# Performance work log

Hardware: AMD Instinct MI355X
Metric: run time of the kernel (lower is better)

## Reference

```python
import jax, jax.numpy as jnp
import numpy as np

B, H, S, DH = 2, 16, 2048, 64
MASK_FILL = -10000.0


def setup_inputs() -> dict:
    key = jax.random.key(0)
    kq, kk, kv = jax.random.split(key, 3)
    q = jax.random.normal(kq, (B, H, S, DH), dtype=jnp.float32)
    k = jax.random.normal(kk, (B, H, S, DH), dtype=jnp.float32)
    v = jax.random.normal(kv, (B, H, S, DH), dtype=jnp.float32)
    # causal mask: True where attention is disallowed (upper triangle)
    mask = jnp.triu(jnp.ones((S, S), dtype=jnp.bool_), k=1)
    return {"q": q, "k": k, "v": v, "mask": mask}


def reference(q, k, v, mask):
    scale = 1.0 / jnp.sqrt(jnp.asarray(k.shape[-1], dtype=q.dtype))
    # scores: [B, H, S_q, S_k]
    scores = jnp.einsum("bhqd,bhkd->bhqk", q, k) * scale
    # additive mask: masked_fill on a zeros [S_k, S_v] matrix -> -10000 where mask
    attn_bias = jnp.where(mask, jnp.asarray(MASK_FILL, dtype=k.dtype),
                          jnp.asarray(0.0, dtype=k.dtype))
    scores = scores + attn_bias  # broadcast over batch/heads
    attn = jax.nn.softmax(scores, axis=-1)
    # dropout_rate = 0.0 -> identity
    return jnp.einsum("bhqk,bhkd->bhqd", attn, v)
```

## Files before the change

kernel.cpp:

```cpp
#include <hip/hip_runtime.h>


#define S_LEN  2048
#define DHDIM  64
#define NHEADS 32
#define LDP    72
#define M2     23.083120654223414f
#define QSCALE 0.18033688011117658f

typedef __attribute__((ext_vector_type(8))) short bf16x8;
typedef __attribute__((ext_vector_type(4))) float f32x4;

__device__ __forceinline__ unsigned short f2bf(float f) {
    unsigned u = __float_as_uint(f);
    return (unsigned short)((u + 0x7fffu + ((u >> 16) & 1u)) >> 16);
}
__device__ __forceinline__ void ld8(const float* p, float* f) {
    float4 a = *(const float4*)p, b = *(const float4*)(p + 4);
    f[0]=a.x; f[1]=a.y; f[2]=a.z; f[3]=a.w; f[4]=b.x; f[5]=b.y; f[6]=b.z; f[7]=b.w;
}
__device__ __forceinline__ uint4 pack8(const float* f, float scale) {
    union { uint4 v; unsigned short s[8]; } w;
    #pragma unroll
    for (int j = 0; j < 8; j++) w.s[j] = f2bf(f[j] * scale);
    return w.v;
}
__device__ __forceinline__ unsigned packhi(float a, float b) {
#if __has_builtin(__builtin_amdgcn_perm)
    return __builtin_amdgcn_perm(__float_as_uint(b), __float_as_uint(a), 0x07060302u);
#else
    return (__float_as_uint(a) >> 16) | (__float_as_uint(b) & 0xffff0000u);
#endif
}

__global__ __launch_bounds__(256) void prep(
    const float* __restrict__ Qf, const float* __restrict__ Kf,
    const float* __restrict__ Vf, unsigned short* __restrict__ qb,
    unsigned short* __restrict__ kb, unsigned short* __restrict__ vtb)
{
    const int st = blockIdx.x, bh = blockIdx.y;
    __shared__ unsigned short lt[64][LDP];
    const float* vp = Vf + ((size_t)bh * S_LEN + st * 64) * DHDIM;
    for (int c = threadIdx.x; c < 512; c += 256) {
        int s = c >> 3, d0 = (c & 7) * 8;
        float f[8]; ld8(vp + s * DHDIM + d0, f);
        #pragma unroll
        for (int j = 0; j < 8; j++) lt[d0 + j][s] = f2bf(f[j]);
    }
    size_t off = ((size_t)(bh * 32 + st) * 4096) + (size_t)threadIdx.x * 16;
    float f[8];
    ld8(Qf + off, f);     *(uint4*)(qb + off)     = pack8(f, QSCALE);
    ld8(Qf + off + 8, f); *(uint4*)(qb + off + 8) = pack8(f, QSCALE);
    ld8(Kf + off, f);     *(uint4*)(kb + off)     = pack8(f, 1.0f);
    ld8(Kf + off + 8, f); *(uint4*)(kb + off + 8) = pack8(f, 1.0f);
    __syncthreads();
    unsigned short* op = vtb + (size_t)bh * DHDIM * S_LEN + st * 64;
    for (int c = threadIdx.x; c < 512; c += 256) {
        int d = c >> 3, s0 = (c & 7) * 8;
        *(uint4*)(op + (size_t)d * S_LEN + s0) = *(const uint4*)&lt[d][s0];
    }
}

template <bool PRE>
__global__ __launch_bounds__(256) void fattn_kernel(
    const void* __restrict__ Qp, const void* __restrict__ Kp,
    const void* __restrict__ Vp, float* __restrict__ O)
{
    __shared__ unsigned short smem[192 * LDP];
    unsigned short (*ks)[LDP]  = (unsigned short(*)[LDP])smem;
    unsigned short (*vts)[LDP] = (unsigned short(*)[LDP])(smem + 64 * LDP);
    unsigned short (*qs)[LDP]  = (unsigned short(*)[LDP])(smem + 128 * LDP);
    unsigned short (*pst)[LDP] = qs;

    const int id = blockIdx.y * 32 + blockIdx.x;
    const int g  = id >> 8;
    const int r8 = id & 255;
    const int bh = r8 >> 3;
    const int s8 = r8 & 7;
    const int qt = (g == 0) ? 31 - 2 * s8
                 : (g == 1) ? 2 * s8
                 : (g == 2) ? 30 - 2 * s8
                            : 2 * s8 + 1;

    const int tid = threadIdx.x;
    const int wave = tid >> 6, lane = tid & 63;
    const int quad = lane >> 4, l16 = lane & 15;

    if constexpr (PRE) {
        const unsigned short* src = (const unsigned short*)Qp
            + ((size_t)bh * S_LEN + qt * 64) * DHDIM;
        for (int c = tid; c < 512; c += 256) {
            int row = c >> 3, c8 = (c & 7) * 8;
            *(uint4*)&qs[row][c8] = *(const uint4*)(src + row * DHDIM + c8);
        }
    } else {
        const float* src = (const float*)Qp + ((size_t)bh * S_LEN + qt * 64) * DHDIM;
        for (int c = tid; c < 512; c += 256) {
            int row = c >> 3, c8 = (c & 7) * 8;
            float f[8]; ld8(src + row * DHDIM + c8, f);
            *(uint4*)&qs[row][c8] = pack8(f, QSCALE);
        }
    }
    __syncthreads();

    const int prow = wave * 16 + l16;
    const bf16x8 bq0 = *(const bf16x8*)&qs[prow][quad * 8];
    const bf16x8 bq1 = *(const bf16x8*)&qs[prow][32 + quad * 8];

    float l_p = 0.f;
    f32x4 of[4];
    #pragma unroll
    for (int n = 0; n < 4; n++) of[n] = (f32x4){0.f, 0.f, 0.f, 0.f};

    for (int kt = 0; kt <= qt; kt++) {
        __syncthreads();

        if constexpr (PRE) {
            const unsigned short* ksrc = (const unsigned short*)Kp
                + ((size_t)bh * S_LEN + kt * 64) * DHDIM;
            const unsigned short* vsrc = (const unsigned short*)Vp
                + (size_t)bh * DHDIM * S_LEN + kt * 64;
            for (int c = tid; c < 512; c += 256) {
                int row = c >> 3, c8 = (c & 7) * 8;
                *(uint4*)&ks[row][c8]  = *(const uint4*)(ksrc + row * DHDIM + c8);
                *(uint4*)&vts[row][c8] = *(const uint4*)(vsrc + (size_t)row * S_LEN + c8);
            }
        } else {
            const float* ksrc = (const float*)Kp + ((size_t)bh * S_LEN + kt * 64) * DHDIM;
            const float* vsrc = (const float*)Vp + ((size_t)bh * S_LEN + kt * 64) * DHDIM;
            for (int c = tid; c < 512; c += 256) {
                int row = c >> 3, c8 = (c & 7) * 8;
                float f[8];
                ld8(ksrc + row * DHDIM + c8, f);
                *(uint4*)&ks[row][c8] = pack8(f, 1.0f);
                ld8(vsrc + row * DHDIM + c8, f);
                #pragma unroll
                for (int j = 0; j < 8; j++) vts[c8 + j][row] = f2bf(f[j]);
            }
        }
        __syncthreads();

        f32x4 sf[4];
        #pragma unroll
        for (int n = 0; n < 4; n++) {
            bf16x8 ak0 = *(const bf16x8*)&ks[n * 16 + l16][quad * 8];
            bf16x8 ak1 = *(const bf16x8*)&ks[n * 16 + l16][32 + quad * 8];
            sf[n] = (f32x4){-M2, -M2, -M2, -M2};
            sf[n] = __builtin_amdgcn_mfma_f32_16x16x32_bf16(ak0, bq0, sf[n], 0, 0, 0);
            sf[n] = __builtin_amdgcn_mfma_f32_16x16x32_bf16(ak1, bq1, sf[n], 0, 0, 0);
        }

        const bool diag = (kt == qt);
        #pragma unroll
        for (int n = 0; n < 4; n++) {
            float p[4];
            #pragma unroll
            for (int r = 0; r < 4; r++) {
                p[r] = exp2f(sf[n][r]);
                if (diag && (n * 16 + quad * 4 + r > wave * 16 + l16)) p[r] = 0.f;
                l_p += p[r];
            }
            uint2 dw;
            dw.x = packhi(p[0], p[1]);
            dw.y = packhi(p[2], p[3]);
            *(uint2*)&pst[prow][n * 16 + quad * 4] = dw;
        }
        asm volatile("s_waitcnt lgkmcnt(0)" ::: "memory");

        bf16x8 bp0 = *(const bf16x8*)&pst[prow][quad * 8];
        bf16x8 bp1 = *(const bf16x8*)&pst[prow][32 + quad * 8];
        #pragma unroll
        for (int n = 0; n < 4; n++) {
            bf16x8 av0 = *(const bf16x8*)&vts[n * 16 + l16][quad * 8];
            bf16x8 av1 = *(const bf16x8*)&vts[n * 16 + l16][32 + quad * 8];
            of[n] = __builtin_amdgcn_mfma_f32_16x16x32_bf16(av0, bp0, of[n], 0, 0, 0);
            of[n] = __builtin_amdgcn_mfma_f32_16x16x32_bf16(av1, bp1, of[n], 0, 0, 0);
        }
    }

    l_p += __shfl_xor(l_p, 16);
    l_p += __shfl_xor(l_p, 32);
    const float inv = 1.f / l_p;
    float* op = O + ((size_t)bh * S_LEN + qt * 64 + wave * 16 + l16) * DHDIM;
    #pragma unroll
    for (int n = 0; n < 4; n++) {
        float4 o4 = make_float4(of[n][0] * inv, of[n][1] * inv,
                                of[n][2] * inv, of[n][3] * inv);
        *(float4*)(op + n * 16 + quad * 4) = o4;
    }
}

extern "C" void kernel_launch(void* const* d_in, const int* in_sizes, int n_in,
                              void* d_out, int out_size, void* d_ws, size_t ws_size,
                              hipStream_t stream) {
    const float* Q = (const float*)d_in[0];
    const float* K = (const float*)d_in[1];
    const float* V = (const float*)d_in[2];
    float* O = (float*)d_out;
    const size_t N = (size_t)NHEADS * S_LEN * DHDIM;

    if (ws_size >= 3 * N * sizeof(unsigned short) && d_ws) {
        unsigned short* qb  = (unsigned short*)d_ws;
        unsigned short* kb  = qb + N;
        unsigned short* vtb = kb + N;
        prep<<<dim3(S_LEN / 64, NHEADS), 256, 0, stream>>>(Q, K, V, qb, kb, vtb);
        fattn_kernel<true><<<dim3(32, 32), 256, 0, stream>>>(qb, kb, vtb, O);
    } else {
        fattn_kernel<false><<<dim3(32, 32), 256, 0, stream>>>(Q, K, V, O);
    }
}
```

Before: 158.6 us.

## Split causal KV range across two blocks and combine partial outputs

Adds a split-K attention path where each query tile's causal key range is divided into two halves processed by separate blocks, writing unnormalized partial outputs and row sums to workspace. A third combine kernel sums the two partials and normalizes them. This doubles the grid to reduce the long tail from the largest diagonal tiles and improve load balance across CUs. The cost is an extra launch plus writing and reading partial buffers. The path only runs when the workspace is large enough, otherwise the original path is used.

```diff
diff --git a/kernel.cpp b/kernel.cpp
--- a/kernel.cpp
+++ b/kernel.cpp
@@ -61,6 +61,131 @@
     }
 }
 
+__global__ __launch_bounds__(256) void fattn_splitk(
+    const unsigned short* __restrict__ Qp, const unsigned short* __restrict__ Kp,
+    const unsigned short* __restrict__ Vp,
+    float* __restrict__ pO, float* __restrict__ pL)
+{
+    __shared__ unsigned short smem[192 * LDP];
+    unsigned short (*ks)[LDP]  = (unsigned short(*)[LDP])smem;
+    unsigned short (*vts)[LDP] = (unsigned short(*)[LDP])(smem + 64 * LDP);
+    unsigned short (*qs)[LDP]  = (unsigned short(*)[LDP])(smem + 128 * LDP);
+    unsigned short (*pst)[LDP] = qs;
+
+    const int id   = blockIdx.y * 64 + blockIdx.x;
+    const int qt   = 31 - (id >> 6);
+    const int rem  = id & 63;
+    const int bh   = rem >> 1;
+    const int half = rem & 1;
+    const int kmid = (qt + 2) >> 1;
+    const int k0   = half ? kmid : 0;
+    const int k1   = half ? qt + 1 : kmid;
+    const int slot = ((bh * 32 + qt) << 1) | half;
+
+    const int tid = threadIdx.x;
+    const int wave = tid >> 6, lane = tid & 63;
+    const int quad = lane >> 4, l16 = lane & 15;
+
+    {
+        const unsigned short* src = Qp + ((size_t)bh * S_LEN + qt * 64) * DHDIM;
+        for (int c = tid; c < 512; c += 256) {
+            int row = c >> 3, c8 = (c & 7) * 8;
+            *(uint4*)&qs[row][c8] = *(const uint4*)(src + row * DHDIM + c8);
+        }
+    }
+    __syncthreads();
+
+    const int prow = wave * 16 + l16;
+    const bf16x8 bq0 = *(const bf16x8*)&qs[prow][quad * 8];
+    const bf16x8 bq1 = *(const bf16x8*)&qs[prow][32 + quad * 8];
+
+    float l_p = 0.f;
+    f32x4 of[4];
+    #pragma unroll
+    for (int n = 0; n < 4; n++) of[n] = (f32x4){0.f, 0.f, 0.f, 0.f};
+
+    for (int kt = k0; kt < k1; kt++) {
+        __syncthreads();
+
+        const unsigned short* ksrc = Kp + ((size_t)bh * S_LEN + kt * 64) * DHDIM;
+        const unsigned short* vsrc = Vp + (size_t)bh * DHDIM * S_LEN + kt * 64;
+        for (int c = tid; c < 512; c += 256) {
+            int row = c >> 3, c8 = (c & 7) * 8;
+            *(uint4*)&ks[row][c8]  = *(const uint4*)(ksrc + row * DHDIM + c8);
+            *(uint4*)&vts[row][c8] = *(const uint4*)(vsrc + (size_t)row * S_LEN + c8);
+        }
+        __syncthreads();
+
+        f32x4 sf[4];
+        #pragma unroll
+        for (int n = 0; n < 4; n++) {
+            bf16x8 ak0 = *(const bf16x8*)&ks[n * 16 + l16][quad * 8];
+            bf16x8 ak1 = *(const bf16x8*)&ks[n * 16 + l16][32 + quad * 8];
+            sf[n] = (f32x4){-M2, -M2, -M2, -M2};
+            sf[n] = __builtin_amdgcn_mfma_f32_16x16x32_bf16(ak0, bq0, sf[n], 0, 0, 0);
+            sf[n] = __builtin_amdgcn_mfma_f32_16x16x32_bf16(ak1, bq1, sf[n], 0, 0, 0);
+        }
+
+        const bool diag = (kt == qt);
+        #pragma unroll
+        for (int n = 0; n < 4; n++) {
+            float p[4];
+            #pragma unroll
+            for (int r = 0; r < 4; r++) {
+                p[r] = exp2f(sf[n][r]);
+                if (diag && (n * 16 + quad * 4 + r > prow)) p[r] = 0.f;
+                l_p += p[r];
+            }
+            uint2 dw;
+            dw.x = packhi(p[0], p[1]);
+            dw.y = packhi(p[2], p[3]);
+            *(uint2*)&pst[prow][n * 16 + quad * 4] = dw;
+        }
+        asm volatile("s_waitcnt lgkmcnt(0)" ::: "memory");
+
+        bf16x8 bp0 = *(const bf16x8*)&pst[prow][quad * 8];
+        bf16x8 bp1 = *(const bf16x8*)&pst[prow][32 + quad * 8];
+        #pragma unroll
+        for (int n = 0; n < 4; n++) {
+            bf16x8 av0 = *(const bf16x8*)&vts[n * 16 + l16][quad * 8];
+            bf16x8 av1 = *(const bf16x8*)&vts[n * 16 + l16][32 + quad * 8];
+            of[n] = __builtin_amdgcn_mfma_f32_16x16x32_bf16(av0, bp0, of[n], 0, 0, 0);
+            of[n] = __builtin_amdgcn_mfma_f32_16x16x32_bf16(av1, bp1, of[n], 0, 0, 0);
+        }
+    }
+
+    l_p += __shfl_xor(l_p, 16);
+    l_p += __shfl_xor(l_p, 32);
+    if (quad == 0) pL[slot * 64 + prow] = l_p;
+    float* op = pO + (size_t)slot * 4096 + prow * 64;
+    #pragma unroll
+    for (int n = 0; n < 4; n++)
+        *(float4*)(op + n * 16 + quad * 4) =
+            make_float4(of[n][0], of[n][1], of[n][2], of[n][3]);
+}
+
+__global__ __launch_bounds__(256) void combine(
+    const float* __restrict__ pO, const float* __restrict__ pL,
+    float* __restrict__ O)
+{
+    const int qt = blockIdx.x, bh = blockIdx.y;
+    const int sa = ((bh * 32 + qt) << 1), sb = sa | 1;
+    const float* A = pO + (size_t)sa * 4096;
+    const float* B = pO + (size_t)sb * 4096;
+    float* out = O + ((size_t)bh * S_LEN + qt * 64) * DHDIM;
+    #pragma unroll
+    for (int k = 0; k < 4; k++) {
+        int c = threadIdx.x + k * 256;
+        int row = c >> 4;
+        float inv = 1.f / (pL[sa * 64 + row] + pL[sb * 64 + row]);
+        float4 a = *(const float4*)(A + c * 4);
+        float4 b = *(const float4*)(B + c * 4);
+        *(float4*)(out + c * 4) = make_float4(
+            (a.x + b.x) * inv, (a.y + b.y) * inv,
+            (a.z + b.z) * inv, (a.w + b.w) * inv);
+    }
+}
+
 template <bool PRE>
 __global__ __launch_bounds__(256) void fattn_kernel(
     const void* __restrict__ Qp, const void* __restrict__ Kp,
@@ -77,10 +202,8 @@
     const int r8 = id & 255;
     const int bh = r8 >> 3;
     const int s8 = r8 & 7;
-    const int qt = (g == 0) ? 31 - 2 * s8
-                 : (g == 1) ? 2 * s8
-                 : (g == 2) ? 30 - 2 * s8
-                            : 2 * s8 + 1;
+    const int qt = (g == 0) ? 31 - 2 * s8 : (g == 1) ? 2 * s8
+                 : (g == 2) ? 30 - 2 * s8 : 2 * s8 + 1;
 
     const int tid = threadIdx.x;
     const int wave = tid >> 6, lane = tid & 63;
@@ -114,7 +237,6 @@
 
     for (int kt = 0; kt <= qt; kt++) {
         __syncthreads();
-
         if constexpr (PRE) {
             const unsigned short* ksrc = (const unsigned short*)Kp
                 + ((size_t)bh * S_LEN + kt * 64) * DHDIM;
@@ -157,7 +279,7 @@
             #pragma unroll
             for (int r = 0; r < 4; r++) {
                 p[r] = exp2f(sf[n][r]);
-                if (diag && (n * 16 + quad * 4 + r > wave * 16 + l16)) p[r] = 0.f;
+                if (diag && (n * 16 + quad * 4 + r > prow)) p[r] = 0.f;
                 l_p += p[r];
             }
             uint2 dw;
@@ -181,13 +303,11 @@
     l_p += __shfl_xor(l_p, 16);
     l_p += __shfl_xor(l_p, 32);
     const float inv = 1.f / l_p;
-    float* op = O + ((size_t)bh * S_LEN + qt * 64 + wave * 16 + l16) * DHDIM;
-    #pragma unroll
-    for (int n = 0; n < 4; n++) {
-        float4 o4 = make_float4(of[n][0] * inv, of[n][1] * inv,
-                                of[n][2] * inv, of[n][3] * inv);
-        *(float4*)(op + n * 16 + quad * 4) = o4;
-    }
+    float* op = O + ((size_t)bh * S_LEN + qt * 64 + prow) * DHDIM;
+    #pragma unroll
+    for (int n = 0; n < 4; n++)
+        *(float4*)(op + n * 16 + quad * 4) = make_float4(
+            of[n][0] * inv, of[n][1] * inv, of[n][2] * inv, of[n][3] * inv);
 }
 
 extern "C" void kernel_launch(void* const* d_in, const int* in_sizes, int n_in,
@@ -198,8 +318,19 @@
     const float* V = (const float*)d_in[2];
     float* O = (float*)d_out;
     const size_t N = (size_t)NHEADS * S_LEN * DHDIM;
-
-    if (ws_size >= 3 * N * sizeof(unsigned short) && d_ws) {
+    const size_t prepB  = 3 * N * sizeof(unsigned short);
+    const size_t partB  = (size_t)2048 * (4096 + 64) * sizeof(float);
+
+    if (d_ws && ws_size >= prepB + partB) {
+        unsigned short* qb  = (unsigned short*)d_ws;
+        unsigned short* kb  = qb + N;
+        unsigned short* vtb = kb + N;
+        float* pO = (float*)((char*)d_ws + prepB);
+        float* pL = pO + (size_t)2048 * 4096;
+        prep<<<dim3(S_LEN / 64, NHEADS), 256, 0, stream>>>(Q, K, V, qb, kb, vtb);
+        fattn_splitk<<<dim3(64, 32), 256, 0, stream>>>(qb, kb, vtb, pO, pL);
+        combine<<<dim3(32, 32), 256, 0, stream>>>(pO, pL, O);
+    } else if (d_ws && ws_size >= prepB) {
         unsigned short* qb  = (unsigned short*)d_ws;
         unsigned short* kb  = qb + N;
         unsigned short* vtb = kb + N;
```

After: 148.0 us. 6.7% less time.
